# Kernel tuning notes

Hardware: AMD Instinct MI355X
Metric: run time of the kernel (lower is better)

Reference implementation:

```python
import jax, jax.numpy as jnp
import numpy as np

B, S, E, HID, NTR, NCAL, CW, VOCAB, POS = 4096, 201, 32, 512, 4, 8, 16, 32, 256
LN_EPS = 1e-5


def _ln(x, g, b):
    m = x.mean(-1, keepdims=True)
    v = ((x - m) ** 2).mean(-1, keepdims=True)
    return (x - m) * jax.lax.rsqrt(v + LN_EPS) * g + b


def setup_inputs() -> dict:
    key = jax.random.key(0)
    ks = jax.random.split(key, 24)
    g = lambda i, shape, s=0.1: (jax.random.normal(ks[i], shape, jnp.float32) * s)
    return dict(
        encoded_seq=jax.random.randint(ks[0], (B, S), 0, VOCAB, jnp.int32),
        experiment_id=jax.random.randint(ks[1], (B,), 0, NCAL, jnp.int32),
        tok_emb=g(2, (VOCAB, E), 1.0),
        pos_emb=g(3, (POS, E), 1.0),
        ln1_g=jnp.ones((NTR, E)), ln1_b=jnp.zeros((NTR, E)),
        wq=g(4, (NTR, E, E)), wk=g(5, (NTR, E, E)), wv=g(6, (NTR, E, E)),
        bq=g(7, (NTR, E), 0.01), bk=g(8, (NTR, E), 0.01), bv=g(9, (NTR, E), 0.01),
        wo=g(10, (NTR, E, E)), bo=g(11, (NTR, E), 0.01),
        ln2_g=jnp.ones((NTR, E)), ln2_b=jnp.zeros((NTR, E)),
        w1=g(12, (NTR, E, HID)), b1=g(13, (NTR, HID), 0.01),
        w2=g(14, (NTR, HID, E)), b2=g(15, (NTR, E), 0.01),
        lnf_g=jnp.ones((E,)), lnf_b=jnp.zeros((E,)),
        wpen=g(16, (E, 1)), bpen=g(17, (1,), 0.01),
        wfan=g(18, (1, CW)), bfan=g(19, (CW,), 0.01),
        wcal=g(20, (NCAL, CW, 1)), bcal=g(21, (NCAL, 1), 0.01),
    )


def reference(encoded_seq, experiment_id, tok_emb, pos_emb,
              ln1_g, ln1_b, wq, wk, wv, bq, bk, bv, wo, bo,
              ln2_g, ln2_b, w1, b1, w2, b2,
              lnf_g, lnf_b, wpen, bpen, wfan, bfan, wcal, bcal):
    # embedding + positional add: [B,S,E]
    x = tok_emb[encoded_seq] + pos_emb[jnp.arange(S)]
    scale = 1.0 / jnp.sqrt(jnp.float32(E))  # num_heads=1 => head_dim=E
    for i in range(NTR):
        n = _ln(x, ln1_g[i], ln1_b[i])
        q = n @ wq[i] + bq[i]
        k = n @ wk[i] + bk[i]
        v = n @ wv[i] + bv[i]
        a = jax.nn.softmax(jnp.einsum('bqe,bke->bqk', q, k) * scale, axis=-1)
        att = jnp.einsum('bqk,bke->bqe', a, v) @ wo[i] + bo[i]
        x = x + att
        h = _ln(x, ln2_g[i], ln2_b[i])
        x = x + (jax.nn.silu(h @ w1[i] + b1[i]) @ w2[i] + b2[i])
    contrib = _ln(x, lnf_g, lnf_b) @ wpen + bpen        # [B,S,1]
    underlying = contrib.sum(axis=-2)                    # [B,1]
    pre = jax.nn.elu(underlying @ wfan + bfan)           # [B,CW]
    # all calibrator heads at once: [B,NCAL]
    all_corr = jnp.einsum('bc,ncj->bn', pre, wcal) + bcal[:, 0]
    mask = jax.nn.one_hot(experiment_id, NCAL, dtype=pre.dtype)  # exactly the (exp==id) mask-sum
    corrected = (all_corr * mask).sum(-1, keepdims=True) + underlying
    return corrected.squeeze()
```

## Files before the change

kernel.cpp:

```cpp
#include <hip/hip_runtime.h>


#define SS   201
#define SP   208
#define NMT  13
#define EE   32
#define HIDN 512
#define NTRL 4
#define CWN  16
#define BB   4096
#define XST  36
#define QST  36
#define MST  72
#define VWST 228

#define X_OFF    0
#define K_OFF    14976
#define VWT_OFF  29952
#define QS_OFF   44544
#define MS_OFF   49152
#define RS_OFF   49984
#define BIAS_OFF 50816
#define SMEM_SZ  51840

#define WS_FRAG  0
#define WS_BIAS  294912
#define WS_B1    299008
#define WS_FIN   307200
#define L2E      1.4426950408889634f

typedef unsigned short u16;
typedef unsigned int   u32;
typedef short bf16x4 __attribute__((ext_vector_type(4)));
typedef short bf16x8 __attribute__((ext_vector_type(8)));
typedef float f32x4  __attribute__((ext_vector_type(4)));
typedef float f32x2  __attribute__((ext_vector_type(2)));

#define CBAR asm volatile("" ::: "memory")

__device__ __forceinline__ f32x4 MF(bf16x8 a, bf16x8 b, f32x4 c){
  return __builtin_amdgcn_mfma_f32_16x16x32_bf16(a, b, c, 0, 0, 0);
}
__device__ __forceinline__ float bf2f(u16 u){ return __uint_as_float(((u32)u)<<16); }
__device__ __forceinline__ u16 f2bf(float f){
  u32 u = __float_as_uint(f);
  u += 0x7fffu + ((u>>16)&1u);
  return (u16)(u>>16);
}
__device__ __forceinline__ u16 f2bf_fast(float f){
  return (u16)((__float_as_uint(f) + 0x8000u) >> 16);
}
__device__ __forceinline__ u32 pk2bf(f32x2 v){
#if defined(__has_builtin) && __has_builtin(__builtin_amdgcn_cvt_pk_bf16_f32)
  auto r = __builtin_amdgcn_cvt_pk_bf16_f32(v.x, v.y);
  u32 u; __builtin_memcpy(&u, &r, 4); return u;
#else
  return ((__float_as_uint(v.x)+0x8000u)>>16) | ((__float_as_uint(v.y)+0x8000u) & 0xffff0000u);
#endif
}
__device__ __forceinline__ f32x2 upk2(u32 d){
  return f32x2{ __uint_as_float(d<<16), __uint_as_float(d & 0xffff0000u) };
}
template<bool F32>
__device__ __forceinline__ float ldv(const void* p, int i){
  if (F32) return ((const float*)p)[i];
  return bf2f(((const u16*)p)[i]);
}
template<bool F32>
__device__ __forceinline__ u16 ldbf(const void* p, int i){
  if (F32) return f2bf(((const float*)p)[i]);
  return ((const u16*)p)[i];
}
__device__ __forceinline__ bf16x8 ld8(const u16* p){
  const bf16x4* q = (const bf16x4*)p;
  bf16x4 lo = q[0], hi = q[1];
  bf16x8 r = {lo[0],lo[1],lo[2],lo[3],hi[0],hi[1],hi[2],hi[3]};
  return r;
}
__device__ __forceinline__ bf16x8 cat44(bf16x4 lo, bf16x4 hi){
  bf16x8 r = {lo[0],lo[1],lo[2],lo[3],hi[0],hi[1],hi[2],hi[3]};
  return r;
}
__device__ __forceinline__ bf16x8 mk8(u32 a0, u32 a1, u32 a2, u32 a3){
  u32 t[4] = {a0,a1,a2,a3};
  bf16x8 r; __builtin_memcpy(&r, t, 16); return r;
}

__device__ __forceinline__ int sniff_bf16(const void* tok_emb, int tid){
  int sane = 0;
  if (tid < 64){
    u16 wd = ((const u16*)tok_emb)[tid];
    int e = (wd >> 7) & 0xFF;
    sane = (e >= 100 && e <= 140) ? 1 : 0;
  }
  return (__syncthreads_count(sane) >= 52) ? 1 : 0;
}

template<bool F32>
__device__ __forceinline__ void frag_body(const void* wq, const void* wk,
    const void* wv, const void* wo, const void* w1, const void* w2, void* ws)
{
  int t = blockIdx.x;
  int l = t / 72, k = t % 72;
  int lane = threadIdx.x, l16 = lane & 15, quad = lane >> 4;
  bf16x8 v;
  if (k < 8){
    int mat = k >> 1, half = k & 1;
    if (mat == 2){
      int col = half*16 + l16;
      #pragma unroll
      for (int j=0;j<8;j++){
        int a = quad*8 + j;
        float acc = 0.f;
        for (int e=0;e<EE;e++)
          acc += ldv<F32>(wv, l*1024 + a*32 + e) * ldv<F32>(wo, l*1024 + e*32 + col);
        v[j] = (short)f2bf(acc);
      }
    } else {
      const void* src = (mat==0)? wq : (mat==1)? wk : wo;
      #pragma unroll
      for (int j=0;j<8;j++)
        v[j] = (short)ldbf<F32>(src, l*1024 + (quad*8+j)*32 + half*16 + l16);
    }
  } else if (k < 40){
    int nt = k - 8;
    #pragma unroll
    for (int j=0;j<8;j++)
      v[j] = (short)ldbf<F32>(w1, l*16384 + (quad*8+j)*512 + nt*16 + l16);
  } else {
    int kc = (k-40)>>1, nh = (k-40)&1;
    #pragma unroll
    for (int j=0;j<8;j++)
      v[j] = (short)ldbf<F32>(w2, l*16384 + (kc*32+quad*8+j)*32 + nh*16 + l16);
  }
  *(bf16x8*)((char*)ws + WS_FRAG + t*1024 + lane*16) = v;
}

__global__ __launch_bounds__(64) void fmt_frags(
    const void* __restrict__ tok_emb,
    const void* __restrict__ wq, const void* __restrict__ wk,
    const void* __restrict__ wv, const void* __restrict__ wo,
    const void* __restrict__ w1, const void* __restrict__ w2,
    void* __restrict__ ws)
{
  if (sniff_bf16(tok_emb, threadIdx.x)) frag_body<false>(wq,wk,wv,wo,w1,w2,ws);
  else                                  frag_body<true >(wq,wk,wv,wo,w1,w2,ws);
}

template<bool F32>
__device__ __forceinline__ void bias_body(
    const void* bq, const void* bk, const void* bv, const void* wo, const void* bo,
    const void* ln1_g, const void* ln1_b, const void* ln2_g, const void* ln2_b,
    const void* b1, const void* b2,
    const void* lnf_g, const void* lnf_b, const void* wpen, const void* bpen,
    const void* wfan, const void* bfan, const void* wcal, const void* bcal,
    void* ws)
{
  int tid = threadIdx.x, idx = tid & 31, grp = tid >> 5;
  float* BW  = (float*)((char*)ws + WS_BIAS);
  float* BW1 = (float*)((char*)ws + WS_B1);
  float* FW  = (float*)((char*)ws + WS_FIN);
  for (int l=0;l<NTRL;l++){
    float v = 0.f;
    switch(grp){
      case 0: v = ldv<F32>(bq, l*32+idx); break;
      case 1: v = ldv<F32>(bk, l*32+idx); break;
      case 2: {
        float acc = ldv<F32>(bo, l*32+idx);
        for (int e=0;e<EE;e++) acc += ldv<F32>(bv, l*32+e) * ldv<F32>(wo, l*1024 + e*32 + idx);
        v = acc; break;
      }
      case 3: v = ldv<F32>(ln1_g, l*32+idx); break;
      case 4: v = ldv<F32>(ln1_b, l*32+idx); break;
      case 5: v = ldv<F32>(ln2_g, l*32+idx); break;
      case 6: v = ldv<F32>(ln2_b, l*32+idx); break;
      case 7: v = ldv<F32>(b2,   l*32+idx); break;
    }
    BW[l*256 + tid] = v;
  }
  for (int i=tid; i<NTRL*HIDN; i+=256) BW1[i] = ldv<F32>(b1, i);
  if (tid < 32){
    FW[tid]    = ldv<F32>(lnf_g, tid);
    FW[32+tid] = ldv<F32>(lnf_b, tid);
    FW[64+tid] = ldv<F32>(wpen, tid);
  }
  if (tid == 0) FW[96] = ldv<F32>(bpen, 0);
  if (tid < 16){ FW[97+tid] = ldv<F32>(wfan, tid); FW[113+tid] = ldv<F32>(bfan, tid); }
  if (tid < 128) FW[129+tid] = ldv<F32>(wcal, tid);
  if (tid < 8)   FW[257+tid] = ldv<F32>(bcal, tid);
}

__global__ __launch_bounds__(256) void fmt_bias(
    const void* __restrict__ tok_emb,
    const void* __restrict__ bq, const void* __restrict__ bk,
    const void* __restrict__ bv, const void* __restrict__ wo, const void* __restrict__ bo,
    const void* __restrict__ ln1_g, const void* __restrict__ ln1_b,
    const void* __restrict__ ln2_g, const void* __restrict__ ln2_b,
    const void* __restrict__ b1, const void* __restrict__ b2,
    const void* __restrict__ lnf_g, const void* __restrict__ lnf_b,
    const void* __restrict__ wpen, const void* __restrict__ bpen,
    const void* __restrict__ wfan, const void* __restrict__ bfan,
    const void* __restrict__ wcal, const void* __restrict__ bcal,
    void* __restrict__ ws)
{
  if (sniff_bf16(tok_emb, threadIdx.x))
    bias_body<false>(bq,bk,bv,wo,bo,ln1_g,ln1_b,ln2_g,ln2_b,b1,b2,
                     lnf_g,lnf_b,wpen,bpen,wfan,bfan,wcal,bcal,ws);
  else
    bias_body<true >(bq,bk,bv,wo,bo,ln1_g,ln1_b,ln2_g,ln2_b,b1,b2,
                     lnf_g,lnf_b,wpen,bpen,wfan,bfan,wcal,bcal,ws);
}

__device__ __forceinline__ void ln_stats(const u16* Xb, float* MS, float* RS, int tid){
  if (tid < SP){
    const u32* row = (const u32*)(Xb + tid*XST);
    f32x2 v[16]; f32x2 s2 = {0.f,0.f};
    #pragma unroll
    for (int i=0;i<16;i++){ f32x2 p = upk2(row[i]); v[i] = p; s2 += p; }
    float m = (s2.x + s2.y) * (1.f/EE);
    f32x2 m2 = {m, m};
    f32x2 var2 = {0.f,0.f};
    #pragma unroll
    for (int i=0;i<16;i++){ f32x2 d = v[i]-m2; var2 += d*d; }
    MS[tid] = m;
    RS[tid] = rsqrtf((var2.x+var2.y)*(1.f/EE) + 1e-5f);
  }
}

__device__ __forceinline__ bf16x8 build_nfrag(const u16* Xb, const float* MS, const float* RS,
                                              int row, int quad, const f32x2* G2, const f32x2* B2){
  const u32* raw = (const u32*)(Xb + row*XST + quad*8);
  f32x2 m2 = { MS[row], MS[row] };
  f32x2 rs2 = { RS[row], RS[row] };
  u32 o[4];
  #pragma unroll
  for (int p=0;p<4;p++){
    f32x2 x = upk2(raw[p]);
    o[p] = pk2bf((x - m2) * rs2 * G2[p] + B2[p]);
  }
  bf16x8 r; __builtin_memcpy(&r, o, 16);
  return r;
}

template<bool F32>
__device__ __forceinline__ void tr_body(
    const int* seq, const int* expid,
    const void* tok_emb, const void* pos_emb,
    const void* ws, void* out, unsigned char* smem)
{
  u16*   Xb   = (u16*)(smem + X_OFF);
  u16*   Kb   = (u16*)(smem + K_OFF);
  u16*   VWTb = (u16*)(smem + VWT_OFF);
  u16*   QSb  = (u16*)(smem + QS_OFF);
  float* MS   = (float*)(smem + MS_OFF);
  float* RS   = (float*)(smem + RS_OFF);
  float* BIAS = (float*)(smem + BIAS_OFF);

  const int tid  = threadIdx.x;
  const int lane = tid & 63, w = tid >> 6;
  const int l16  = lane & 15, quad = lane >> 4;
  const int b    = blockIdx.x;
  const f32x4 Z  = {0.f,0.f,0.f,0.f};
  u16* qs = QSb + w*576;
  u16* qm = (u16*)(smem + VWT_OFF) + w*1152;

  {
    const int* srow = seq + b*SS;
    for (int i = tid; i < SP*EE; i += 256){
      int s = i >> 5, e = i & 31;
      float val = 0.f;
      if (s < SS){
        int tok = srow[s];
        val = ldv<F32>(tok_emb, tok*EE + e) + ldv<F32>(pos_emb, s*EE + e);
      }
      Xb[s*XST + e] = f2bf(val);
    }
  }
  __syncthreads();

  const float qce = 0.2550546813f;
  const f32x2 qce2 = {qce, qce};
  const f32x2 one2 = {1.f, 1.f};
  const f32x2 nl2e2 = {-L2E, -L2E};

  for (int l = 0; l < NTRL; ++l){
    const char* wsl = (const char*)ws + WS_FRAG + l*73728;
    bf16x8 bwq0 = *(const bf16x8*)(wsl + 0*1024 + lane*16);
    bf16x8 bwq1 = *(const bf16x8*)(wsl + 1*1024 + lane*16);
    bf16x8 bwk0 = *(const bf16x8*)(wsl + 2*1024 + lane*16);
    bf16x8 bwk1 = *(const bf16x8*)(wsl + 3*1024 + lane*16);
    bf16x8 bwv0 = *(const bf16x8*)(wsl + 4*1024 + lane*16);
    bf16x8 bwv1 = *(const bf16x8*)(wsl + 5*1024 + lane*16);
    {
      const float* BW = (const float*)((const char*)ws + WS_BIAS) + l*256;
      BIAS[tid] = BW[tid];
    }
    for (int i = tid; i < 32*16; i += 256)
      VWTb[(i>>4)*VWST + 208 + (i&15)] = 0;
    ln_stats(Xb, MS, RS, tid);
    __syncthreads();

    bf16x8 aq[4];
    {
      f32x2 G2[4], B2[4];
      #pragma unroll
      for (int p=0;p<4;p++){
        G2[p] = f32x2{BIAS[96+quad*8+2*p], BIAS[96+quad*8+2*p+1]};
        B2[p] = f32x2{BIAS[128+quad*8+2*p], BIAS[128+quad*8+2*p+1]};
      }
      f32x2 bqb2 = {BIAS[l16],    BIAS[16+l16]};
      f32x2 bkb2 = {BIAS[32+l16], BIAS[48+l16]};
      #pragma unroll
      for (int t=0;t<4;t++){
        int m = w + 4*t;
        if (m < NMT){
          int m16 = m*16;
          bf16x8 an = build_nfrag(Xb, MS, RS, m16+l16, quad, G2, B2);
          f32x4 ck0 = MF(an, bwk0, Z), ck1 = MF(an, bwk1, Z);
          #pragma unroll
          for (int r=0;r<4;r++){
            int row = m16 + quad*4 + r;
            u32 pk = pk2bf(f32x2{ck0[r], ck1[r]} + bkb2);
            Kb[row*XST + l16]      = (u16)pk;
            Kb[row*XST + 16 + l16] = (u16)(pk>>16);
          }
          f32x4 cw0 = MF(an, bwv0, Z), cw1 = MF(an, bwv1, Z);
          #pragma unroll
          for (int r=0;r<4;r++){
            u32 pk = pk2bf(f32x2{cw0[r], cw1[r]});
            VWTb[l16*VWST      + m16 + quad*4 + r] = (u16)pk;
            VWTb[(16+l16)*VWST + m16 + quad*4 + r] = (u16)(pk>>16);
          }
          f32x4 cq0 = MF(an, bwq0, Z), cq1 = MF(an, bwq1, Z);
          #pragma unroll
          for (int r=0;r<4;r++){
            u32 pk = pk2bf((f32x2{cq0[r], cq1[r]} + bqb2) * qce2);
            qs[(quad*4+r)*QST + l16]      = (u16)pk;
            qs[(quad*4+r)*QST + 16 + l16] = (u16)(pk>>16);
          }
          CBAR;
          aq[t] = ld8(qs + l16*QST + quad*8);
          CBAR;
        }
      }
    }
    __syncthreads();

    {
      const u16* vbase0 = VWTb + l16*VWST;
      const u16* vbase1 = VWTb + (16+l16)*VWST;
      f32x4 ob0 = *(const f32x4*)(BIAS + 64 + quad*4);
      f32x4 ob1 = *(const f32x4*)(BIAS + 80 + quad*4);
      #pragma unroll
      for (int t=0;t<4;t++){
        int m = w + 4*t;
        if (m < NMT){
          int m16 = m*16;
          u32 pbw[13][2];
          float part = 0.f;
          #pragma unroll
          for (int kt=0; kt<13; kt++){
            bf16x8 kb8 = ld8(Kb + (kt*16+l16)*XST + quad*8);
            f32x4 St = MF(kb8, aq[t], Z);
            float e0 = __builtin_amdgcn_exp2f(St[0]);
            float e1 = __builtin_amdgcn_exp2f(St[1]);
            float e2 = __builtin_amdgcn_exp2f(St[2]);
            float e3 = __builtin_amdgcn_exp2f(St[3]);
            if (kt == 12){
              int kb = quad*4;
              if (kb+0 >= 9) e0 = 0.f;
              if (kb+1 >= 9) e1 = 0.f;
              if (kb+2 >= 9) e2 = 0.f;
              if (kb+3 >= 9) e3 = 0.f;
            }
            part += (e0+e1)+(e2+e3);
            pbw[kt][0] = pk2bf(f32x2{e0,e1});
            pbw[kt][1] = pk2bf(f32x2{e2,e3});
          }
          part += __shfl_xor(part, 16);
          part += __shfl_xor(part, 32);
          float inv = __builtin_amdgcn_rcpf(part);

          f32x4 o0 = Z, o1 = Z;
          #pragma unroll
          for (int c=0;c<6;c++){
            bf16x4 a0l = *(const bf16x4*)(vbase0 + c*32 + quad*4);
            bf16x4 a0h = *(const bf16x4*)(vbase0 + c*32 + 16 + quad*4);
            bf16x4 a1l = *(const bf16x4*)(vbase1 + c*32 + quad*4);
            bf16x4 a1h = *(const bf16x4*)(vbase1 + c*32 + 16 + quad*4);
            bf16x8 B8 = mk8(pbw[2*c][0], pbw[2*c][1], pbw[2*c+1][0], pbw[2*c+1][1]);
            o0 = MF(cat44(a0l, a0h), B8, o0);
            o1 = MF(cat44(a1l, a1h), B8, o1);
          }
          {
            bf16x4 a0l = *(const bf16x4*)(vbase0 + 192 + quad*4);
            bf16x4 a0h = *(const bf16x4*)(vbase0 + 208 + quad*4);
            bf16x4 a1l = *(const bf16x4*)(vbase1 + 192 + quad*4);
            bf16x4 a1h = *(const bf16x4*)(vbase1 + 208 + quad*4);
            bf16x8 B8 = mk8(pbw[12][0], pbw[12][1], 0u, 0u);
            o0 = MF(cat44(a0l, a0h), B8, o0);
            o1 = MF(cat44(a1l, a1h), B8, o1);
          }

          u32* xr = (u32*)(Xb + (m16+l16)*XST);
          {
            u32 d0 = xr[quad*2], d1 = xr[quad*2+1];
            f32x2 r01 = f32x2{o0[0],o0[1]} * inv + (upk2(d0) + f32x2{ob0[0],ob0[1]});
            f32x2 r23 = f32x2{o0[2],o0[3]} * inv + (upk2(d1) + f32x2{ob0[2],ob0[3]});
            xr[quad*2]   = pk2bf(r01);
            xr[quad*2+1] = pk2bf(r23);
            u32 d2 = xr[8+quad*2], d3 = xr[8+quad*2+1];
            f32x2 s01 = f32x2{o1[0],o1[1]} * inv + (upk2(d2) + f32x2{ob1[0],ob1[1]});
            f32x2 s23 = f32x2{o1[2],o1[3]} * inv + (upk2(d3) + f32x2{ob1[2],ob1[3]});
            xr[8+quad*2]   = pk2bf(s01);
            xr[8+quad*2+1] = pk2bf(s23);
          }
        }
      }
    }
    __syncthreads();

    ln_stats(Xb, MS, RS, tid);
    __syncthreads();

    {
      f32x2 G2[4], B2[4];
      #pragma unroll
      for (int p=0;p<4;p++){
        G2[p] = f32x2{BIAS[160+quad*8+2*p], BIAS[160+quad*8+2*p+1]};
        B2[p] = f32x2{BIAS[192+quad*8+2*p], BIAS[192+quad*8+2*p+1]};
      }
      bf16x8 anc[4];
      #pragma unroll
      for (int t=0;t<4;t++){
        int m = w + 4*t;
        if (m < NMT) anc[t] = build_nfrag(Xb, MS, RS, m*16+l16, quad, G2, B2);
      }
      f32x4 oacc[4][2];
      #pragma unroll
      for (int t=0;t<4;t++){ oacc[t][0] = Z; oacc[t][1] = Z; }
      const char* w1f = wsl + 8*1024;
      const char* w2f = wsl + 40*1024;
      const float* BW1 = (const float*)((const char*)ws + WS_B1) + l*HIDN;

      for (int hc = 0; hc < HIDN; hc += 64){
        bf16x8 bw1[4], bw2[2][2];
        #pragma unroll
        for (int nt=0;nt<4;nt++)
          bw1[nt] = *(const bf16x8*)(w1f + (hc/16 + nt)*1024 + lane*16);
        #pragma unroll
        for (int kc=0;kc<2;kc++){
          bw2[kc][0] = *(const bf16x8*)(w2f + ((hc/32 + kc)*2    )*1024 + lane*16);
          bw2[kc][1] = *(const bf16x8*)(w2f + ((hc/32 + kc)*2 + 1)*1024 + lane*16);
        }
        f32x2 b1v2[4];
        #pragma unroll
        for (int nt=0;nt<4;nt++){
          float bb = BW1[hc + nt*16 + l16];
          b1v2[nt] = f32x2{bb, bb};
        }
        #pragma unroll
        for (int t=0;t<4;t++){
          int m = w + 4*t;
          if (m < NMT){
            #pragma unroll
            for (int nt=0;nt<4;nt++){
              f32x4 h = MF(anc[t], bw1[nt], Z);
              #pragma unroll
              for (int rp=0;rp<2;rp++){
                f32x2 z = f32x2{h[2*rp], h[2*rp+1]} + b1v2[nt];
                f32x2 a = z * nl2e2;
                f32x2 e = { __builtin_amdgcn_exp2f(a.x), __builtin_amdgcn_exp2f(a.y) };
                f32x2 d = one2 + e;
                f32x2 rc = { __builtin_amdgcn_rcpf(d.x), __builtin_amdgcn_rcpf(d.y) };
                f32x2 s = z * rc;
                u32 pk = pk2bf(s);
                qm[(quad*4+2*rp  )*MST + nt*16 + l16] = (u16)pk;
                qm[(quad*4+2*rp+1)*MST + nt*16 + l16] = (u16)(pk>>16);
              }
            }
            CBAR;
            bf16x8 ah0 = ld8(qm + l16*MST + quad*8);
            bf16x8 ah1 = ld8(qm + l16*MST + 32 + quad*8);
            oacc[t][0] = MF(ah0, bw2[0][0], oacc[t][0]);
            oacc[t][0] = MF(ah1, bw2[1][0], oacc[t][0]);
            oacc[t][1] = MF(ah0, bw2[0][1], oacc[t][1]);
            oacc[t][1] = MF(ah1, bw2[1][1], oacc[t][1]);
            CBAR;
          }
        }
      }

      f32x2 b2v2 = {BIAS[224+l16], BIAS[240+l16]};
      #pragma unroll
      for (int t=0;t<4;t++){
        int m = w + 4*t;
        if (m < NMT){
          int m16 = m*16;
          #pragma unroll
          for (int r=0;r<4;r++){
            int row = m16 + quad*4 + r;
            u16* x0 = Xb + row*XST + l16;
            u16* x1 = Xb + row*XST + 16 + l16;
            f32x2 xv = { bf2f(*x0), bf2f(*x1) };
            f32x2 ov = f32x2{oacc[t][0][r], oacc[t][1][r]} + (xv + b2v2);
            u32 pk = pk2bf(ov);
            *x0 = (u16)pk; *x1 = (u16)(pk>>16);
          }
        }
      }
    }
    __syncthreads();
  }

  const float* FW = (const float*)((const char*)ws + WS_FIN);
  if (tid < 32){
    BIAS[tid]    = FW[tid];
    BIAS[32+tid] = FW[32+tid];
    BIAS[64+tid] = FW[64+tid];
  }
  __syncthreads();
  float part = 0.f;
  if (tid < SS){
    const u32* row = (const u32*)(Xb + tid*XST);
    f32x2 v[16]; f32x2 s2 = {0.f,0.f};
    #pragma unroll
    for (int i=0;i<16;i++){ f32x2 p = upk2(row[i]); v[i] = p; s2 += p; }
    float m = (s2.x+s2.y) * (1.f/EE);
    f32x2 m2 = {m,m};
    f32x2 var2 = {0.f,0.f};
    #pragma unroll
    for (int i=0;i<16;i++){ f32x2 d = v[i]-m2; var2 += d*d; }
    float rs = rsqrtf((var2.x+var2.y)*(1.f/EE) + 1e-5f);
    f32x2 rs2 = {rs, rs};
    f32x2 dot2 = {0.f,0.f};
    #pragma unroll
    for (int i=0;i<16;i++){
      f32x2 g  = {BIAS[2*i], BIAS[2*i+1]};
      f32x2 bb = {BIAS[32+2*i], BIAS[33+2*i]};
      f32x2 wp = {BIAS[64+2*i], BIAS[65+2*i]};
      dot2 += ((v[i]-m2)*rs2*g + bb) * wp;
    }
    part = dot2.x + dot2.y + FW[96];
  }
  #pragma unroll
  for (int off=32; off; off>>=1) part += __shfl_xor(part, off);
  float* REDF = (float*)(smem + QS_OFF);
  __syncthreads();
  if (lane == 0) REDF[w] = part;
  __syncthreads();
  if (tid == 0){
    float u = REDF[0] + REDF[1] + REDF[2] + REDF[3];
    int ex = expid[b];
    float corr = FW[257+ex];
    #pragma unroll
    for (int c = 0; c < CWN; ++c){
      float pre = u * FW[97+c] + FW[113+c];
      pre = pre > 0.f ? pre : (__expf(pre) - 1.f);
      corr += pre * FW[129 + ex*CWN + c];
    }
    float res = corr + u;
    if (F32) ((float*)out)[b] = res;
    else     ((u16*)out)[b]  = f2bf(res);
  }
}

__global__ __launch_bounds__(256, 3) void tr_kernel(
    const int* __restrict__ seq, const int* __restrict__ expid,
    const void* __restrict__ tok_emb, const void* __restrict__ pos_emb,
    const void* __restrict__ ws, void* __restrict__ out)
{
  __shared__ __align__(16) unsigned char smem[SMEM_SZ];
  if (sniff_bf16(tok_emb, threadIdx.x))
    tr_body<false>(seq, expid, tok_emb, pos_emb, ws, out, smem);
  else
    tr_body<true >(seq, expid, tok_emb, pos_emb, ws, out, smem);
}

extern "C" void kernel_launch(void* const* d_in, const int* in_sizes, int n_in,
                              void* d_out, int out_size, void* d_ws, size_t ws_size,
                              hipStream_t stream)
{
  (void)in_sizes; (void)n_in; (void)ws_size; (void)out_size;
  const void* tok_emb = d_in[2];
  fmt_frags<<<dim3(288), dim3(64), 0, stream>>>(
      tok_emb, d_in[6], d_in[7], d_in[8], d_in[12], d_in[16], d_in[18], d_ws);
  fmt_bias<<<dim3(1), dim3(256), 0, stream>>>(
      tok_emb, d_in[9], d_in[10], d_in[11], d_in[12], d_in[13],
      d_in[4], d_in[5], d_in[14], d_in[15], d_in[17], d_in[19],
      d_in[20], d_in[21], d_in[22], d_in[23],
      d_in[24], d_in[25], d_in[26], d_in[27], d_ws);
  tr_kernel<<<dim3(BB), dim3(256), 0, stream>>>(
      (const int*)d_in[0], (const int*)d_in[1], tok_emb, d_in[3], d_ws, d_out);
}
```

Before: 924.2 us.

## Transpose MFMA operands so outputs feed next MFMA directly from registers

The Q projection and the MLP up-projection now compute transposed products (weights as the A operand, activations as B). Each lane's accumulator then already holds the K-contiguous elements the next MFMA needs, so the LDS round-trip through per-wave scratch buffers (qs/qm) and its compiler barriers are removed. The w2 fragment layout is permuted to match the new hidden-dim ordering, K reads are split into two 4-element loads, and the residual write-back uses packed 32-bit LDS accesses. This trades shared-memory stores and loads for register-only packing, at the risk of layout mismatches between the fragment prep and the consumer.

```diff
diff --git a/kernel.cpp b/kernel.cpp
--- a/kernel.cpp
+++ b/kernel.cpp
@@ -10,8 +10,6 @@
 #define CWN  16
 #define BB   4096
 #define XST  36
-#define QST  36
-#define MST  72
 #define VWST 228
 
 #define X_OFF    0
@@ -36,8 +34,6 @@
 typedef float f32x4  __attribute__((ext_vector_type(4)));
 typedef float f32x2  __attribute__((ext_vector_type(2)));
 
-#define CBAR asm volatile("" ::: "memory")
-
 __device__ __forceinline__ f32x4 MF(bf16x8 a, bf16x8 b, f32x4 c){
   return __builtin_amdgcn_mfma_f32_16x16x32_bf16(a, b, c, 0, 0, 0);
 }
@@ -46,9 +42,6 @@
   u32 u = __float_as_uint(f);
   u += 0x7fffu + ((u>>16)&1u);
   return (u16)(u>>16);
-}
-__device__ __forceinline__ u16 f2bf_fast(float f){
-  return (u16)((__float_as_uint(f) + 0x8000u) >> 16);
 }
 __device__ __forceinline__ u32 pk2bf(f32x2 v){
 #if defined(__has_builtin) && __has_builtin(__builtin_amdgcn_cvt_pk_bf16_f32)
@@ -71,12 +64,6 @@
   if (F32) return f2bf(((const float*)p)[i]);
   return ((const u16*)p)[i];
 }
-__device__ __forceinline__ bf16x8 ld8(const u16* p){
-  const bf16x4* q = (const bf16x4*)p;
-  bf16x4 lo = q[0], hi = q[1];
-  bf16x8 r = {lo[0],lo[1],lo[2],lo[3],hi[0],hi[1],hi[2],hi[3]};
-  return r;
-}
 __device__ __forceinline__ bf16x8 cat44(bf16x4 lo, bf16x4 hi){
   bf16x8 r = {lo[0],lo[1],lo[2],lo[3],hi[0],hi[1],hi[2],hi[3]};
   return r;
@@ -84,6 +71,13 @@
 __device__ __forceinline__ bf16x8 mk8(u32 a0, u32 a1, u32 a2, u32 a3){
   u32 t[4] = {a0,a1,a2,a3};
   bf16x8 r; __builtin_memcpy(&r, t, 16); return r;
+}
+__device__ __forceinline__ u32 silu_pk(float za, float zb){
+  float ea = __builtin_amdgcn_exp2f(za * -L2E);
+  float eb = __builtin_amdgcn_exp2f(zb * -L2E);
+  float ra = __builtin_amdgcn_rcpf(1.f + ea);
+  float rb = __builtin_amdgcn_rcpf(1.f + eb);
+  return pk2bf(f32x2{za*ra, zb*rb});
 }
 
 __device__ __forceinline__ int sniff_bf16(const void* tok_emb, int tid){
@@ -130,8 +124,10 @@
   } else {
     int kc = (k-40)>>1, nh = (k-40)&1;
     #pragma unroll
-    for (int j=0;j<8;j++)
-      v[j] = (short)ldbf<F32>(w2, l*16384 + (kc*32+quad*8+j)*32 + nh*16 + l16);
+    for (int j=0;j<8;j++){
+      int hh = kc*32 + ((j&4) ? 16 : 0) + quad*4 + (j&3);
+      v[j] = (short)ldbf<F32>(w2, l*16384 + hh*32 + nh*16 + l16);
+    }
   }
   *(bf16x8*)((char*)ws + WS_FRAG + t*1024 + lane*16) = v;
 }
@@ -251,7 +247,6 @@
   u16*   Xb   = (u16*)(smem + X_OFF);
   u16*   Kb   = (u16*)(smem + K_OFF);
   u16*   VWTb = (u16*)(smem + VWT_OFF);
-  u16*   QSb  = (u16*)(smem + QS_OFF);
   float* MS   = (float*)(smem + MS_OFF);
   float* RS   = (float*)(smem + RS_OFF);
   float* BIAS = (float*)(smem + BIAS_OFF);
@@ -261,8 +256,6 @@
   const int l16  = lane & 15, quad = lane >> 4;
   const int b    = blockIdx.x;
   const f32x4 Z  = {0.f,0.f,0.f,0.f};
-  u16* qs = QSb + w*576;
-  u16* qm = (u16*)(smem + VWT_OFF) + w*1152;
 
   {
     const int* srow = seq + b*SS;
@@ -279,9 +272,7 @@
   __syncthreads();
 
   const float qce = 0.2550546813f;
-  const f32x2 qce2 = {qce, qce};
-  const f32x2 one2 = {1.f, 1.f};
-  const f32x2 nl2e2 = {-L2E, -L2E};
+  const f32x4 qce4 = {qce, qce, qce, qce};
 
   for (int l = 0; l < NTRL; ++l){
     const char* wsl = (const char*)ws + WS_FRAG + l*73728;
@@ -308,8 +299,9 @@
         G2[p] = f32x2{BIAS[96+quad*8+2*p], BIAS[96+quad*8+2*p+1]};
         B2[p] = f32x2{BIAS[128+quad*8+2*p], BIAS[128+quad*8+2*p+1]};
       }
-      f32x2 bqb2 = {BIAS[l16],    BIAS[16+l16]};
       f32x2 bkb2 = {BIAS[32+l16], BIAS[48+l16]};
+      f32x4 bq0 = *(const f32x4*)(BIAS + quad*4);
+      f32x4 bq1 = *(const f32x4*)(BIAS + 16 + quad*4);
       #pragma unroll
       for (int t=0;t<4;t++){
         int m = w + 4*t;
@@ -331,16 +323,11 @@
             VWTb[l16*VWST      + m16 + quad*4 + r] = (u16)pk;
             VWTb[(16+l16)*VWST + m16 + quad*4 + r] = (u16)(pk>>16);
           }
-          f32x4 cq0 = MF(an, bwq0, Z), cq1 = MF(an, bwq1, Z);
-          #pragma unroll
-          for (int r=0;r<4;r++){
-            u32 pk = pk2bf((f32x2{cq0[r], cq1[r]} + bqb2) * qce2);
-            qs[(quad*4+r)*QST + l16]      = (u16)pk;
-            qs[(quad*4+r)*QST + 16 + l16] = (u16)(pk>>16);
-          }
-          CBAR;
-          aq[t] = ld8(qs + l16*QST + quad*8);
-          CBAR;
+          f32x4 cq0 = MF(bwq0, an, Z), cq1 = MF(bwq1, an, Z);
+          f32x4 z0 = (cq0 + bq0) * qce4;
+          f32x4 z1 = (cq1 + bq1) * qce4;
+          aq[t] = mk8(pk2bf(f32x2{z0[0], z0[1]}), pk2bf(f32x2{z0[2], z0[3]}),
+                      pk2bf(f32x2{z1[0], z1[1]}), pk2bf(f32x2{z1[2], z1[3]}));
         }
       }
     }
@@ -360,7 +347,9 @@
           float part = 0.f;
           #pragma unroll
           for (int kt=0; kt<13; kt++){
-            bf16x8 kb8 = ld8(Kb + (kt*16+l16)*XST + quad*8);
+            const u16* krow = Kb + (kt*16+l16)*XST;
+            bf16x8 kb8 = cat44(*(const bf16x4*)(krow + quad*4),
+                               *(const bf16x4*)(krow + 16 + quad*4));
             f32x4 St = MF(kb8, aq[t], Z);
             float e0 = __builtin_amdgcn_exp2f(St[0]);
             float e1 = __builtin_amdgcn_exp2f(St[1]);
@@ -443,70 +432,44 @@
       const char* w2f = wsl + 40*1024;
       const float* BW1 = (const float*)((const char*)ws + WS_B1) + l*HIDN;
 
-      for (int hc = 0; hc < HIDN; hc += 64){
-        bf16x8 bw1[4], bw2[2][2];
-        #pragma unroll
-        for (int nt=0;nt<4;nt++)
-          bw1[nt] = *(const bf16x8*)(w1f + (hc/16 + nt)*1024 + lane*16);
-        #pragma unroll
-        for (int kc=0;kc<2;kc++){
-          bw2[kc][0] = *(const bf16x8*)(w2f + ((hc/32 + kc)*2    )*1024 + lane*16);
-          bw2[kc][1] = *(const bf16x8*)(w2f + ((hc/32 + kc)*2 + 1)*1024 + lane*16);
-        }
-        f32x2 b1v2[4];
-        #pragma unroll
-        for (int nt=0;nt<4;nt++){
-          float bb = BW1[hc + nt*16 + l16];
-          b1v2[nt] = f32x2{bb, bb};
-        }
+      for (int hp = 0; hp < 16; ++hp){
+        bf16x8 a1lo = *(const bf16x8*)(w1f + (2*hp  )*1024 + lane*16);
+        bf16x8 a1hi = *(const bf16x8*)(w1f + (2*hp+1)*1024 + lane*16);
+        bf16x8 a2e0 = *(const bf16x8*)(w2f + (hp*2  )*1024 + lane*16);
+        bf16x8 a2e1 = *(const bf16x8*)(w2f + (hp*2+1)*1024 + lane*16);
+        f32x4 b1q0 = *(const f32x4*)(BW1 + hp*32      + quad*4);
+        f32x4 b1q1 = *(const f32x4*)(BW1 + hp*32 + 16 + quad*4);
         #pragma unroll
         for (int t=0;t<4;t++){
           int m = w + 4*t;
           if (m < NMT){
-            #pragma unroll
-            for (int nt=0;nt<4;nt++){
-              f32x4 h = MF(anc[t], bw1[nt], Z);
-              #pragma unroll
-              for (int rp=0;rp<2;rp++){
-                f32x2 z = f32x2{h[2*rp], h[2*rp+1]} + b1v2[nt];
-                f32x2 a = z * nl2e2;
-                f32x2 e = { __builtin_amdgcn_exp2f(a.x), __builtin_amdgcn_exp2f(a.y) };
-                f32x2 d = one2 + e;
-                f32x2 rc = { __builtin_amdgcn_rcpf(d.x), __builtin_amdgcn_rcpf(d.y) };
-                f32x2 s = z * rc;
-                u32 pk = pk2bf(s);
-                qm[(quad*4+2*rp  )*MST + nt*16 + l16] = (u16)pk;
-                qm[(quad*4+2*rp+1)*MST + nt*16 + l16] = (u16)(pk>>16);
-              }
-            }
-            CBAR;
-            bf16x8 ah0 = ld8(qm + l16*MST + quad*8);
-            bf16x8 ah1 = ld8(qm + l16*MST + 32 + quad*8);
-            oacc[t][0] = MF(ah0, bw2[0][0], oacc[t][0]);
-            oacc[t][0] = MF(ah1, bw2[1][0], oacc[t][0]);
-            oacc[t][1] = MF(ah0, bw2[0][1], oacc[t][1]);
-            oacc[t][1] = MF(ah1, bw2[1][1], oacc[t][1]);
-            CBAR;
+            f32x4 z0 = MF(a1lo, anc[t], Z) + b1q0;
+            f32x4 z1 = MF(a1hi, anc[t], Z) + b1q1;
+            bf16x8 H8 = mk8(silu_pk(z0[0], z0[1]), silu_pk(z0[2], z0[3]),
+                            silu_pk(z1[0], z1[1]), silu_pk(z1[2], z1[3]));
+            oacc[t][0] = MF(a2e0, H8, oacc[t][0]);
+            oacc[t][1] = MF(a2e1, H8, oacc[t][1]);
           }
         }
       }
 
-      f32x2 b2v2 = {BIAS[224+l16], BIAS[240+l16]};
+      f32x4 b2q0 = *(const f32x4*)(BIAS + 224 + quad*4);
+      f32x4 b2q1 = *(const f32x4*)(BIAS + 240 + quad*4);
       #pragma unroll
       for (int t=0;t<4;t++){
         int m = w + 4*t;
         if (m < NMT){
-          int m16 = m*16;
-          #pragma unroll
-          for (int r=0;r<4;r++){
-            int row = m16 + quad*4 + r;
-            u16* x0 = Xb + row*XST + l16;
-            u16* x1 = Xb + row*XST + 16 + l16;
-            f32x2 xv = { bf2f(*x0), bf2f(*x1) };
-            f32x2 ov = f32x2{oacc[t][0][r], oacc[t][1][r]} + (xv + b2v2);
-            u32 pk = pk2bf(ov);
-            *x0 = (u16)pk; *x1 = (u16)(pk>>16);
-          }
+          u32* xr = (u32*)(Xb + (m*16 + l16)*XST);
+          u32 d0 = xr[quad*2], d1 = xr[quad*2+1];
+          f32x2 r01 = f32x2{oacc[t][0][0], oacc[t][0][1]} + (upk2(d0) + f32x2{b2q0[0], b2q0[1]});
+          f32x2 r23 = f32x2{oacc[t][0][2], oacc[t][0][3]} + (upk2(d1) + f32x2{b2q0[2], b2q0[3]});
+          xr[quad*2]   = pk2bf(r01);
+          xr[quad*2+1] = pk2bf(r23);
+          u32 d2 = xr[8+quad*2], d3 = xr[8+quad*2+1];
+          f32x2 s01 = f32x2{oacc[t][1][0], oacc[t][1][1]} + (upk2(d2) + f32x2{b2q1[0], b2q1[1]});
+          f32x2 s23 = f32x2{oacc[t][1][2], oacc[t][1][3]} + (upk2(d3) + f32x2{b2q1[2], b2q1[3]});
+          xr[8+quad*2]   = pk2bf(s01);
+          xr[8+quad*2+1] = pk2bf(s23);
         }
       }
     }
```

Result: slower. 951.8 us (+3.0%).
